# Kernel tuning notes

Hardware: AMD Instinct MI355X
Metric: run time of the kernel (lower is better)

The kernel has to match this reference:

```python
import jax, jax.numpy as jnp
import numpy as np

D_MODEL, N_HEAD, D_HEAD = 192, 16, 6
INNER = N_HEAD * D_HEAD  # 96
LN_EPS = 1e-9
INF = 1e6


def _rel_pos_embeds(S):
    # Funnel get_position_embeds, relative_shift path, block 0
    half = D_MODEL // 2
    freq = jnp.arange(half, dtype=jnp.float32)
    inv_freq = 1.0 / (10000.0 ** (freq / half))
    rel_pos_id = jnp.arange(-2 * S, 2 * S, dtype=jnp.float32)  # [4S]
    sinusoid = rel_pos_id[:, None] * inv_freq[None, :]          # [4S, half]
    pos_embed = jnp.concatenate([jnp.sin(sinusoid), jnp.cos(sinusoid)], axis=-1)  # [4S, D]
    # block 0: relative_pos(pos, stride=1) = arange(S, -S, -1), offset by 2S
    idx = jnp.arange(S, -S, -1) + 2 * S  # [2S]
    return pos_embed[idx]  # [2S, D]


def _relative_shift_gather(pos_attn, context_len):
    # shift = 1 (q_len == context_len)
    B, n, S, M = pos_attn.shape  # M = 2*S
    pa = pos_attn.reshape(B, n, M, S)[:, :, 1:, :]
    pa = pa.reshape(B, n, S, M - 1)[..., :context_len]
    return pa


def setup_inputs() -> dict:
    key = jax.random.key(0)
    ks = jax.random.split(key, 12)
    B, S = 4, 1024
    s = 0.02
    return {
        "x": jax.random.normal(ks[0], (B, S, D_MODEL), dtype=jnp.float32),
        "mask0": jnp.ones((B, S), dtype=jnp.float32),
        "Wq": jax.random.normal(ks[1], (D_MODEL, INNER), dtype=jnp.float32) * s,
        "Wk": jax.random.normal(ks[2], (D_MODEL, INNER), dtype=jnp.float32) * s,
        "bk": jnp.zeros((INNER,), dtype=jnp.float32),
        "Wv": jax.random.normal(ks[3], (D_MODEL, INNER), dtype=jnp.float32) * s,
        "bv": jnp.zeros((INNER,), dtype=jnp.float32),
        "Wo": jax.random.normal(ks[4], (INNER, D_MODEL), dtype=jnp.float32) * s,
        "bo": jnp.zeros((D_MODEL,), dtype=jnp.float32),
        "r_w_bias": jax.random.normal(ks[5], (N_HEAD, D_HEAD), dtype=jnp.float32) * s,
        "r_r_bias": jax.random.normal(ks[6], (N_HEAD, D_HEAD), dtype=jnp.float32) * s,
        "r_kernel": jax.random.normal(ks[7], (D_MODEL, N_HEAD, D_HEAD), dtype=jnp.float32) * s,
        "gamma": jnp.ones((D_MODEL,), dtype=jnp.float32),
        "beta": jnp.zeros((D_MODEL,), dtype=jnp.float32),
    }


def reference(x, mask0, Wq, Wk, bk, Wv, bv, Wo, bo, r_w_bias, r_r_bias, r_kernel, gamma, beta):
    B, S, _ = x.shape
    scale = 1.0 / np.sqrt(D_HEAD).astype(np.float32)

    q = (x @ Wq).reshape(B, S, N_HEAD, D_HEAD) * scale       # q_head pre-scaled
    k = (x @ Wk + bk).reshape(B, S, N_HEAD, D_HEAD)
    v = (x @ Wv + bv).reshape(B, S, N_HEAD, D_HEAD)

    # content score
    content = jnp.einsum("bind,bjnd->bnij", q + r_w_bias * scale, k)

    # positional score with relative shift
    r = _rel_pos_embeds(S)                                    # [2S, D]
    r_head = jnp.einsum("td,dnh->tnh", r, r_kernel)           # [2S, n, h]
    pos_attn = jnp.einsum("binh,tnh->bnit", q + r_r_bias * scale, r_head)  # [B,n,S,2S]
    pos_attn = _relative_shift_gather(pos_attn, S)            # [B,n,S,S]

    attn_score = content + pos_attn  # token_type_attn = 0 (no token_type_ids)
    attn_score = attn_score - INF * (1.0 - mask0[:, None, None, :])
    attn_prob = jax.nn.softmax(attn_score, axis=-1)

    attn_vec = jnp.einsum("bnij,bjnd->bind", attn_prob, v)    # [B,S,n,h]
    attn_out = attn_vec.reshape(B, S, INNER) @ Wo + bo

    h = x + attn_out
    mu = jnp.mean(h, axis=-1, keepdims=True)
    var = jnp.mean(jnp.square(h - mu), axis=-1, keepdims=True)
    out = (h - mu) / jnp.sqrt(var + LN_EPS) * gamma + beta
    return out
```

## Files before the change

kernel.cpp:

```cpp
#include <hip/hip_runtime.h>
#include <hip/hip_bf16.h>
#include <math.h>

#define LOG2E 1.4426950408889634f
#define IS6   0.4082482904638630f

typedef _Float16 h2 __attribute__((ext_vector_type(2)));

#if defined(__has_builtin)
#if __has_builtin(__builtin_amdgcn_fdot2)
#define FDOT2(a,b,c) __builtin_amdgcn_fdot2((a),(b),(c),false)
#endif
#if __has_builtin(__builtin_amdgcn_exp2f)
#define EXP2(x) __builtin_amdgcn_exp2f(x)
#endif
#endif
#ifndef FDOT2
#define FDOT2(a,b,c) ((float)(a).x*(float)(b).x + (float)(a).y*(float)(b).y + (c))
#endif
#ifndef EXP2
#define EXP2(x) exp2f(x)
#endif

__device__ __forceinline__ unsigned packh2(float x, float y) {
    h2 v; v.x = (_Float16)x; v.y = (_Float16)y;
    return *(unsigned*)&v;
}
__device__ __forceinline__ h2 ash2(unsigned u) { return *(h2*)&u; }

__global__ __launch_bounds__(96)
void k_wpack(const float* __restrict__ Wq, const float* __restrict__ Wk,
             const float* __restrict__ Wv, unsigned* __restrict__ Whp) {
    int bid = blockIdx.x;
    int mat = bid / 96, dp = bid - mat * 96;
    const float* W = mat == 0 ? Wq : (mat == 1 ? Wk : Wv);
    int c = threadIdx.x;
    float w0 = W[(2 * dp) * 96 + c];
    float w1 = W[(2 * dp + 1) * 96 + c];
    Whp[(mat * 96 + c) * 96 + dp] = packh2(w0, w1);
}

__global__ __launch_bounds__(256)
void k_pre(const float* __restrict__ x, const unsigned* __restrict__ Whp,
           const float* __restrict__ bk, const float* __restrict__ bv,
           const float* __restrict__ rwb, const float* __restrict__ rrb,
           const float* __restrict__ rk,
           unsigned* __restrict__ QWt, unsigned* __restrict__ QRt,
           unsigned* __restrict__ Kpl, unsigned* __restrict__ Vpl,
           unsigned short* __restrict__ phiB) {
    __shared__ unsigned xs[64 * 97];
    __shared__ float rrowS[4 * 192];
    int tid = threadIdx.x;
    if (blockIdx.x < 1152) {
        int rt = blockIdx.x / 18, qb = blockIdx.x - rt * 18;
        int row0 = rt * 64;
        for (int idx = tid; idx < 6144; idx += 256) {
            int r = idx / 96, dpp = idx - r * 96;
            float2 xv = *(const float2*)&x[(size_t)(row0 + r) * 192 + dpp * 2];
            xs[r * 97 + dpp] = packh2(xv.x, xv.y);
        }
        __syncthreads();
        int quad = __builtin_amdgcn_readfirstlane(tid >> 6);
        int sl = tid & 63;
        int cq = qb * 4 + quad;
        int c0 = cq * 4;
        int mat = c0 / 96, col0 = c0 - mat * 96;
        const unsigned* wb0 = Whp + (mat * 96 + col0) * 96;
        const unsigned* wb1 = wb0 + 96;
        const unsigned* wb2 = wb0 + 192;
        const unsigned* wb3 = wb0 + 288;
        const unsigned* xr = xs + sl * 97;
        float a0 = 0.f, a1 = 0.f, a2 = 0.f, a3 = 0.f;
        #pragma unroll 8
        for (int dp = 0; dp < 96; ++dp) {
            h2 xp = ash2(xr[dp]);
            a0 = FDOT2(xp, ash2(wb0[dp]), a0);
            a1 = FDOT2(xp, ash2(wb1[dp]), a1);
            a2 = FDOT2(xp, ash2(wb2[dp]), a2);
            a3 = FDOT2(xp, ash2(wb3[dp]), a3);
        }
        float av[4] = {a0, a1, a2, a3};
        int row = row0 + sl, b = row >> 10, s = row & 1023;
        if (mat == 0) {
            #pragma unroll
            for (int pp = 0; pp < 2; ++pp) {
                int cA = col0 + 2 * pp;
                int pg = cA >> 1;
                int nn = pg / 3, hp = pg - nn * 3;
                int bnn = b * 16 + nn;
                unsigned qw = packh2((av[2*pp]   + rwb[cA])   * (IS6 * LOG2E),
                                     (av[2*pp+1] + rwb[cA+1]) * (IS6 * LOG2E));
                unsigned qr = packh2((av[2*pp]   + rrb[cA])   * (IS6 * LOG2E),
                                     (av[2*pp+1] + rrb[cA+1]) * (IS6 * LOG2E));
                size_t qo = ((size_t)(hp * 64 + bnn) << 10) + s;
                QWt[qo] = qw;
                QRt[qo] = qr;
            }
        } else if (mat == 1) {
            #pragma unroll
            for (int pp = 0; pp < 2; ++pp) {
                int cA = col0 + 2 * pp;
                int pg = cA >> 1;
                int nn = pg / 3, hp = pg - nn * 3;
                int bnn = b * 16 + nn;
                Kpl[((size_t)(hp * 64 + bnn) << 10) + s] =
                    packh2(av[2*pp] + bk[cA], av[2*pp+1] + bk[cA+1]);
            }
        } else {
            #pragma unroll
            for (int pp = 0; pp < 2; ++pp) {
                int cA = col0 + 2 * pp;
                int pg = cA >> 1;
                int nn = pg / 3, hp = pg - nn * 3;
                int bnn = b * 16 + nn;
                Vpl[((size_t)(hp * 64 + bnn) << 10) + s] =
                    packh2(av[2*pp] + bv[cA], av[2*pp+1] + bv[cA+1]);
            }
        }
    } else {
        int t0 = (blockIdx.x - 1152) * 4;
        for (int idx = tid; idx < 768; idx += 256) {
            int tl = idx / 192, d = idx - tl * 192;
            int dd = d < 96 ? d : d - 96;
            float w = exp2f(-(float)dd * 0.13841367062030676f);
            float ang = (float)(1024 - (t0 + tl)) * w;
            rrowS[idx] = (d < 96) ? __sinf(ang) : __cosf(ang);
        }
        __syncthreads();
        if (tid < 192) {
            int c = tid % 96, tg = tid / 96;
            float acc0 = 0.f, acc1 = 0.f;
            #pragma unroll 4
            for (int d = 0; d < 192; ++d) {
                float wv = rk[d * 96 + c];
                acc0 += rrowS[(tg * 2 + 0) * 192 + d] * wv;
                acc1 += rrowS[(tg * 2 + 1) * 192 + d] * wv;
            }
            int n = c / 6, h = c - n * 6;
            _Float16 v0 = (_Float16)acc0, v1 = (_Float16)acc1;
            phiB[(n * 2048 + t0 + tg * 2 + 0) * 8 + h] = *(unsigned short*)&v0;
            phiB[(n * 2048 + t0 + tg * 2 + 1) * 8 + h] = *(unsigned short*)&v1;
            if (tg == 0 && c < 32) {
                int nn = c >> 1, hh = 6 + (c & 1);
                #pragma unroll
                for (int k = 0; k < 4; ++k)
                    phiB[(nn * 2048 + t0 + k) * 8 + hh] = 0;
            }
        }
    }
}

#define SWZ(r) ((r) ^ (((r) >> 3) & 7))
__global__ __launch_bounds__(256, 4)
void k_attn(const unsigned* __restrict__ QWt, const unsigned* __restrict__ QRt,
            const unsigned* __restrict__ Kpl, const unsigned* __restrict__ Vpl,
            const float* __restrict__ mask0,
            const unsigned short* __restrict__ phiB,
            uint4* __restrict__ P) {
    __shared__ uint4 phiS[1088];
    __shared__ uint4 kS[64];
    __shared__ uint4 vS[64];
    int tid = threadIdx.x;
    int jc = blockIdx.x, n = blockIdx.y, b = blockIdx.z;
    int j0 = jc * 64;
    int bn = b * 16 + n;

    const uint4* phg = (const uint4*)phiB + (n * 2048 + j0 + 1);
    for (int r = tid; r < 1087; r += 256) phiS[SWZ(r)] = phg[r];
    if (tid < 64) {
        int j = j0 + tid;
        size_t base = ((size_t)bn << 10) + j;
        unsigned k01 = Kpl[base], k23 = Kpl[base + 65536], k45 = Kpl[base + 131072];
        unsigned v01 = Vpl[base], v23 = Vpl[base + 65536], v45 = Vpl[base + 131072];
        float mt = 1e6f * (mask0[b * 1024 + j] - 1.0f) * LOG2E;
        kS[tid] = make_uint4(k01, k23, k45, __float_as_uint(mt));
        vS[tid] = make_uint4(v01, v23, v45, 0u);
    }
    __syncthreads();

    int iA = tid * 4;
    size_t qb = ((size_t)bn) << 10;
    h2 qw[4][3], qr[4][3];
    #pragma unroll
    for (int q = 0; q < 4; ++q) {
        #pragma unroll
        for (int hp = 0; hp < 3; ++hp) {
            qw[q][hp] = ash2(QWt[(size_t)hp * 65536 + qb + iA + q]);
            qr[q][hp] = ash2(QRt[(size_t)hp * 65536 + qb + iA + q]);
        }
    }
    float den[4] = {0.f, 0.f, 0.f, 0.f};
    float ac[4][6] = {};
    int Cb = 1023 - iA;
    uint4 r1 = phiS[SWZ(Cb - 1)];
    uint4 r2 = phiS[SWZ(Cb - 2)];
    uint4 r3 = phiS[SWZ(Cb - 3)];

    #pragma unroll 4
    for (int jj = 0; jj < 64; ++jj) {
        uint4 K = kS[jj];
        uint4 V = vS[jj];
        uint4 r0 = phiS[SWZ(Cb + jj)];
        float mt = __uint_as_float(K.w);
        uint4 ph[4] = {r0, r1, r2, r3};
        h2 v01 = ash2(V.x), v23 = ash2(V.y), v45 = ash2(V.z);
        #pragma unroll
        for (int q = 0; q < 4; ++q) {
            float sc = FDOT2(ash2(K.x), qw[q][0],
                       FDOT2(ash2(K.y), qw[q][1],
                       FDOT2(ash2(K.z), qw[q][2], mt)));
            sc = FDOT2(ash2(ph[q].x), qr[q][0],
                 FDOT2(ash2(ph[q].y), qr[q][1],
                 FDOT2(ash2(ph[q].z), qr[q][2], sc)));
            float e = EXP2(sc);
            den[q] += e;
            ac[q][0] += e * (float)v01.x; ac[q][1] += e * (float)v01.y;
            ac[q][2] += e * (float)v23.x; ac[q][3] += e * (float)v23.y;
            ac[q][4] += e * (float)v45.x; ac[q][5] += e * (float)v45.y;
        }
        r3 = r2; r2 = r1; r1 = r0;
    }
    size_t pb = ((size_t)(jc * 64 + bn)) << 10;
    #pragma unroll
    for (int q = 0; q < 4; ++q) {
        uint4 st;
        st.x = packh2(den[q], ac[q][0]);
        st.y = packh2(ac[q][1], ac[q][2]);
        st.z = packh2(ac[q][3], ac[q][4]);
        st.w = packh2(ac[q][5], 0.f);
        P[pb + q * 256 + tid] = st;
    }
}

__global__ __launch_bounds__(256)
void k_out(const uint4* __restrict__ P, const float* __restrict__ Wo,
           const float* __restrict__ bo, const float* __restrict__ x,
           const float* __restrict__ gamma, const float* __restrict__ beta,
           float* __restrict__ out) {
    __shared__ unsigned WoS[96 * 96];
    __shared__ float avS[16 * 96];
    int tid = threadIdx.x;
    int row0 = blockIdx.x * 16;
    for (int idx = tid; idx < 9216; idx += 256) {
        int c = idx / 96, pd = idx - c * 96;
        float2 w = *(const float2*)&Wo[c * 192 + pd * 2];
        WoS[idx] = packh2(w.x, w.y);
    }
    {
        int n = tid >> 4, rl = tid & 15;
        int row = row0 + rl, b = row >> 10, i = row & 1023;
        int bn = b * 16 + n;
        int q = i & 3, tt = i >> 2;
        float d = 0.f, s0 = 0.f, s1 = 0.f, s2 = 0.f, s3 = 0.f, s4 = 0.f, s5 = 0.f;
        #pragma unroll
        for (int jjc = 0; jjc < 16; ++jjc) {
            uint4 u = P[(((size_t)(jjc * 64 + bn)) << 10) + q * 256 + tt];
            h2 x0 = ash2(u.x), x1 = ash2(u.y), x2 = ash2(u.z), x3 = ash2(u.w);
            d  += (float)x0.x; s0 += (float)x0.y; s1 += (float)x1.x; s2 += (float)x1.y;
            s3 += (float)x2.x; s4 += (float)x2.y; s5 += (float)x3.x;
        }
        float inv = 1.0f / d;
        float* o = &avS[rl * 96 + n * 6];
        o[0] = s0 * inv; o[1] = s1 * inv; o[2] = s2 * inv;
        o[3] = s3 * inv; o[4] = s4 * inv; o[5] = s5 * inv;
    }
    __syncthreads();

    int lane = tid & 63, wv = tid >> 6;
    bool act = lane < 48;
    int d0 = lane * 4;
    #pragma unroll
    for (int rr = 0; rr < 4; ++rr) {
        int r = wv * 4 + rr, row = row0 + r;
        float ax = 0.f, ay = 0.f, az = 0.f, aw = 0.f;
        if (act) {
            float4 bq = *(const float4*)&bo[d0];
            float4 xq = *(const float4*)&x[(size_t)row * 192 + d0];
            ax = bq.x + xq.x; ay = bq.y + xq.y; az = bq.z + xq.z; aw = bq.w + xq.w;
            for (int c2 = 0; c2 < 96; ++c2) {
                float a = avS[r * 96 + c2];
                uint2 wp = *(uint2*)&WoS[c2 * 96 + lane * 2];
                h2 w0 = ash2(wp.x), w1 = ash2(wp.y);
                ax += a * (float)w0.x; ay += a * (float)w0.y;
                az += a * (float)w1.x; aw += a * (float)w1.y;
            }
        }
        float sum = act ? (ax + ay + az + aw) : 0.f;
        #pragma unroll
        for (int off = 32; off; off >>= 1) sum += __shfl_xor(sum, off, 64);
        float mu = sum * (1.0f / 192.0f);
        float dx = ax - mu, dy = ay - mu, dz = az - mu, dw = aw - mu;
        float vs = act ? (dx * dx + dy * dy + dz * dz + dw * dw) : 0.f;
        #pragma unroll
        for (int off = 32; off; off >>= 1) vs += __shfl_xor(vs, off, 64);
        float rstd = rsqrtf(vs * (1.0f / 192.0f) + 1e-9f);
        if (act) {
            float4 g = *(const float4*)&gamma[d0];
            float4 bb = *(const float4*)&beta[d0];
            float4 rv;
            rv.x = dx * rstd * g.x + bb.x;
            rv.y = dy * rstd * g.y + bb.y;
            rv.z = dz * rstd * g.z + bb.z;
            rv.w = dw * rstd * g.w + bb.w;
            *(float4*)&out[(size_t)row * 192 + d0] = rv;
        }
    }
}

extern "C" void kernel_launch(void* const* d_in, const int* in_sizes, int n_in,
                              void* d_out, int out_size, void* d_ws, size_t ws_size,
                              hipStream_t stream) {
    const float* x        = (const float*)d_in[0];
    const float* mask0    = (const float*)d_in[1];
    const float* Wq       = (const float*)d_in[2];
    const float* Wk       = (const float*)d_in[3];
    const float* bk       = (const float*)d_in[4];
    const float* Wv       = (const float*)d_in[5];
    const float* bv       = (const float*)d_in[6];
    const float* Wo       = (const float*)d_in[7];
    const float* bo       = (const float*)d_in[8];
    const float* rwb      = (const float*)d_in[9];
    const float* rrb      = (const float*)d_in[10];
    const float* r_kernel = (const float*)d_in[11];
    const float* gamma    = (const float*)d_in[12];
    const float* beta     = (const float*)d_in[13];
    float* out = (float*)d_out;

    unsigned* QWt = (unsigned*)d_ws;
    unsigned* QRt = QWt + 196608;
    unsigned* Kpl = QRt + 196608;
    unsigned* Vpl = Kpl + 196608;
    uint4*    P   = (uint4*)(Vpl + 196608);
    unsigned short* phiB = (unsigned short*)(P + 1048576);
    unsigned* Whp = (unsigned*)(phiB + 262144);

    k_wpack<<<288, 96, 0, stream>>>(Wq, Wk, Wv, Whp);
    k_pre<<<1664, 256, 0, stream>>>(x, Whp, bk, bv, rwb, rrb, r_kernel,
                                    QWt, QRt, Kpl, Vpl, phiB);
    k_attn<<<dim3(16, 16, 4), 256, 0, stream>>>(QWt, QRt, Kpl, Vpl, mask0, phiB, P);
    k_out<<<256, 256, 0, stream>>>(P, Wo, bo, x, gamma, beta, out);
}
```

Before: 94.56 us.

## Retile attention to 8 queries per thread with packed half PV accumulation

The attention kernel now assigns 8 query rows per thread (128 threads per block) and splits keys into 32-key chunks, doubling the grid. Each key/phi load from shared memory is reused across more queries, and phi rows are held in a register ring buffer. The PV accumulation moves to packed fp16 multiply-adds, while the denominator stays in fp32. The split-K partial buffer doubles in size, so the output kernel reduces 32 partials instead of 16. This adds more partial-sum traffic and a precision risk from accumulating in fp16.

```diff
diff --git a/kernel.cpp b/kernel.cpp
--- a/kernel.cpp
+++ b/kernel.cpp
@@ -27,6 +27,22 @@
     return *(unsigned*)&v;
 }
 __device__ __forceinline__ h2 ash2(unsigned u) { return *(h2*)&u; }
+__device__ __forceinline__ unsigned ah2(h2 v) { return *(unsigned*)&v; }
+
+#if defined(__has_builtin)
+#if __has_builtin(__builtin_amdgcn_cvt_pkrtz)
+__device__ __forceinline__ h2 pk2(float a, float b) {
+    auto r = __builtin_amdgcn_cvt_pkrtz(a, b);
+    union { decltype(r) f; h2 h; } c; c.f = r; return c.h;
+}
+#define HAVE_PK2 1
+#endif
+#endif
+#ifndef HAVE_PK2
+__device__ __forceinline__ h2 pk2(float a, float b) {
+    h2 v; v.x = (_Float16)a; v.y = (_Float16)b; return v;
+}
+#endif
 
 __global__ __launch_bounds__(96)
 void k_wpack(const float* __restrict__ Wq, const float* __restrict__ Wk,
@@ -150,85 +166,96 @@
     }
 }
 
-#define SWZ(r) ((r) ^ (((r) >> 3) & 7))
-__global__ __launch_bounds__(256, 4)
+#define SWZ8(r) ((r) ^ ((((r) >> 3) ^ ((r) >> 6)) & 7))
+__global__ __launch_bounds__(128, 3)
 void k_attn(const unsigned* __restrict__ QWt, const unsigned* __restrict__ QRt,
             const unsigned* __restrict__ Kpl, const unsigned* __restrict__ Vpl,
             const float* __restrict__ mask0,
             const unsigned short* __restrict__ phiB,
             uint4* __restrict__ P) {
-    __shared__ uint4 phiS[1088];
+    __shared__ uint4 phiS[1056];
     __shared__ uint4 kS[64];
-    __shared__ uint4 vS[64];
+    __shared__ unsigned vS[192];
     int tid = threadIdx.x;
     int jc = blockIdx.x, n = blockIdx.y, b = blockIdx.z;
-    int j0 = jc * 64;
+    int j0 = jc * 32;
     int bn = b * 16 + n;
 
     const uint4* phg = (const uint4*)phiB + (n * 2048 + j0 + 1);
-    for (int r = tid; r < 1087; r += 256) phiS[SWZ(r)] = phg[r];
-    if (tid < 64) {
-        int j = j0 + tid;
+    for (int r = tid; r < 1055; r += 128) phiS[SWZ8(r)] = phg[r];
+    {
+        int r = tid & 31, hf = tid >> 5;
+        int j = j0 + r;
         size_t base = ((size_t)bn << 10) + j;
-        unsigned k01 = Kpl[base], k23 = Kpl[base + 65536], k45 = Kpl[base + 131072];
-        unsigned v01 = Vpl[base], v23 = Vpl[base + 65536], v45 = Vpl[base + 131072];
-        float mt = 1e6f * (mask0[b * 1024 + j] - 1.0f) * LOG2E;
-        kS[tid] = make_uint4(k01, k23, k45, __float_as_uint(mt));
-        vS[tid] = make_uint4(v01, v23, v45, 0u);
+        if (hf == 0) {
+            float mt = 1e6f * (mask0[b * 1024 + j] - 1.0f) * LOG2E;
+            kS[r] = make_uint4(Kpl[base], Kpl[base + 65536], Kpl[base + 131072],
+                               __float_as_uint(mt));
+        } else if (hf == 1) {
+            vS[r * 3 + 0] = Vpl[base];
+            vS[r * 3 + 1] = Vpl[base + 65536];
+            vS[r * 3 + 2] = Vpl[base + 131072];
+        }
     }
     __syncthreads();
 
-    int iA = tid * 4;
-    size_t qb = ((size_t)bn) << 10;
-    h2 qw[4][3], qr[4][3];
-    #pragma unroll
-    for (int q = 0; q < 4; ++q) {
+    int iA = tid * 8;
+    h2 qw[8][3], qr[8][3];
+    #pragma unroll
+    for (int hp = 0; hp < 3; ++hp) {
+        size_t off = (size_t)hp * 65536 + ((size_t)bn << 10) + iA;
+        uint4 qa = *(const uint4*)&QWt[off];
+        uint4 qb2 = *(const uint4*)&QWt[off + 4];
+        qw[0][hp] = ash2(qa.x); qw[1][hp] = ash2(qa.y); qw[2][hp] = ash2(qa.z); qw[3][hp] = ash2(qa.w);
+        qw[4][hp] = ash2(qb2.x); qw[5][hp] = ash2(qb2.y); qw[6][hp] = ash2(qb2.z); qw[7][hp] = ash2(qb2.w);
+        uint4 ra = *(const uint4*)&QRt[off];
+        uint4 rb = *(const uint4*)&QRt[off + 4];
+        qr[0][hp] = ash2(ra.x); qr[1][hp] = ash2(ra.y); qr[2][hp] = ash2(ra.z); qr[3][hp] = ash2(ra.w);
+        qr[4][hp] = ash2(rb.x); qr[5][hp] = ash2(rb.y); qr[6][hp] = ash2(rb.z); qr[7][hp] = ash2(rb.w);
+    }
+
+    float den[8] = {0.f,0.f,0.f,0.f,0.f,0.f,0.f,0.f};
+    h2 zero2; zero2.x = (_Float16)0.f; zero2.y = (_Float16)0.f;
+    h2 ac0[8], ac1[8], ac2[8];
+    #pragma unroll
+    for (int q = 0; q < 8; ++q) { ac0[q] = zero2; ac1[q] = zero2; ac2[q] = zero2; }
+
+    int Cb = 1023 - iA;
+    uint4 ph[8];
+    #pragma unroll
+    for (int q = 1; q < 8; ++q) ph[8 - q] = phiS[SWZ8(Cb - q)];
+
+    #pragma unroll 8
+    for (int jj = 0; jj < 32; ++jj) {
+        uint4 K = kS[jj];
+        unsigned Vx = vS[3 * jj], Vy = vS[3 * jj + 1], Vz = vS[3 * jj + 2];
+        ph[jj & 7] = phiS[SWZ8(Cb + jj)];
+        float mt = __uint_as_float(K.w);
+        h2 v01 = ash2(Vx), v23 = ash2(Vy), v45 = ash2(Vz);
         #pragma unroll
-        for (int hp = 0; hp < 3; ++hp) {
-            qw[q][hp] = ash2(QWt[(size_t)hp * 65536 + qb + iA + q]);
-            qr[q][hp] = ash2(QRt[(size_t)hp * 65536 + qb + iA + q]);
-        }
-    }
-    float den[4] = {0.f, 0.f, 0.f, 0.f};
-    float ac[4][6] = {};
-    int Cb = 1023 - iA;
-    uint4 r1 = phiS[SWZ(Cb - 1)];
-    uint4 r2 = phiS[SWZ(Cb - 2)];
-    uint4 r3 = phiS[SWZ(Cb - 3)];
-
-    #pragma unroll 4
-    for (int jj = 0; jj < 64; ++jj) {
-        uint4 K = kS[jj];
-        uint4 V = vS[jj];
-        uint4 r0 = phiS[SWZ(Cb + jj)];
-        float mt = __uint_as_float(K.w);
-        uint4 ph[4] = {r0, r1, r2, r3};
-        h2 v01 = ash2(V.x), v23 = ash2(V.y), v45 = ash2(V.z);
-        #pragma unroll
-        for (int q = 0; q < 4; ++q) {
+        for (int q = 0; q < 8; ++q) {
+            uint4 p = ph[(jj - q) & 7];
             float sc = FDOT2(ash2(K.x), qw[q][0],
                        FDOT2(ash2(K.y), qw[q][1],
                        FDOT2(ash2(K.z), qw[q][2], mt)));
-            sc = FDOT2(ash2(ph[q].x), qr[q][0],
-                 FDOT2(ash2(ph[q].y), qr[q][1],
-                 FDOT2(ash2(ph[q].z), qr[q][2], sc)));
+            sc = FDOT2(ash2(p.x), qr[q][0],
+                 FDOT2(ash2(p.y), qr[q][1],
+                 FDOT2(ash2(p.z), qr[q][2], sc)));
             float e = EXP2(sc);
             den[q] += e;
-            ac[q][0] += e * (float)v01.x; ac[q][1] += e * (float)v01.y;
-            ac[q][2] += e * (float)v23.x; ac[q][3] += e * (float)v23.y;
-            ac[q][4] += e * (float)v45.x; ac[q][5] += e * (float)v45.y;
-        }
-        r3 = r2; r2 = r1; r1 = r0;
+            h2 e2 = pk2(e, e);
+            ac0[q] += e2 * v01;
+            ac1[q] += e2 * v23;
+            ac2[q] += e2 * v45;
+        }
     }
     size_t pb = ((size_t)(jc * 64 + bn)) << 10;
     #pragma unroll
-    for (int q = 0; q < 4; ++q) {
+    for (int q = 0; q < 8; ++q) {
         uint4 st;
-        st.x = packh2(den[q], ac[q][0]);
-        st.y = packh2(ac[q][1], ac[q][2]);
-        st.z = packh2(ac[q][3], ac[q][4]);
-        st.w = packh2(ac[q][5], 0.f);
-        P[pb + q * 256 + tid] = st;
+        st.x = __float_as_uint(den[q]);
+        st.y = ah2(ac0[q]); st.z = ah2(ac1[q]); st.w = ah2(ac2[q]);
+        P[pb + q * 128 + tid] = st;
     }
 }
 
@@ -250,14 +277,16 @@
         int n = tid >> 4, rl = tid & 15;
         int row = row0 + rl, b = row >> 10, i = row & 1023;
         int bn = b * 16 + n;
-        int q = i & 3, tt = i >> 2;
+        int q = i & 7, tt = i >> 3;
         float d = 0.f, s0 = 0.f, s1 = 0.f, s2 = 0.f, s3 = 0.f, s4 = 0.f, s5 = 0.f;
         #pragma unroll
-        for (int jjc = 0; jjc < 16; ++jjc) {
-            uint4 u = P[(((size_t)(jjc * 64 + bn)) << 10) + q * 256 + tt];
-            h2 x0 = ash2(u.x), x1 = ash2(u.y), x2 = ash2(u.z), x3 = ash2(u.w);
-            d  += (float)x0.x; s0 += (float)x0.y; s1 += (float)x1.x; s2 += (float)x1.y;
-            s3 += (float)x2.x; s4 += (float)x2.y; s5 += (float)x3.x;
+        for (int jjc = 0; jjc < 32; ++jjc) {
+            uint4 u = P[(((size_t)(jjc * 64 + bn)) << 10) + q * 128 + tt];
+            h2 x0 = ash2(u.y), x1 = ash2(u.z), x2 = ash2(u.w);
+            d  += __uint_as_float(u.x);
+            s0 += (float)x0.x; s1 += (float)x0.y;
+            s2 += (float)x1.x; s3 += (float)x1.y;
+            s4 += (float)x2.x; s5 += (float)x2.y;
         }
         float inv = 1.0f / d;
         float* o = &avS[rl * 96 + n * 6];
@@ -331,12 +360,12 @@
     unsigned* Kpl = QRt + 196608;
     unsigned* Vpl = Kpl + 196608;
     uint4*    P   = (uint4*)(Vpl + 196608);
-    unsigned short* phiB = (unsigned short*)(P + 1048576);
+    unsigned short* phiB = (unsigned short*)(P + 2097152);
     unsigned* Whp = (unsigned*)(phiB + 262144);
 
     k_wpack<<<288, 96, 0, stream>>>(Wq, Wk, Wv, Whp);
     k_pre<<<1664, 256, 0, stream>>>(x, Whp, bk, bv, rwb, rrb, r_kernel,
                                     QWt, QRt, Kpl, Vpl, phiB);
-    k_attn<<<dim3(16, 16, 4), 256, 0, stream>>>(QWt, QRt, Kpl, Vpl, mask0, phiB, P);
+    k_attn<<<dim3(32, 16, 4), 128, 0, stream>>>(QWt, QRt, Kpl, Vpl, mask0, phiB, P);
     k_out<<<256, 256, 0, stream>>>(P, Wo, bo, x, gamma, beta, out);
 }
```

After: 113.5 us. 1.2x slower.
